# Optimization experiments

Hardware: AMD Instinct MI355X
Metric: run time of the kernel (lower is better)

## Reference

```python
import jax, jax.numpy as jnp
from jax import lax
import numpy as np

B, H, W = 16, 512, 512
OPENING_R, EROSION_R, DILATION_R = 5, 2, 1
MIN_SIZE, AREA_THRESHOLD = 2000, 300
INF = np.int32(2 ** 30)


def _disk(r):
    # skimage.morphology.disk: x^2 + y^2 <= r^2 on a (2r+1)^2 grid
    y, x = np.mgrid[-r:r + 1, -r:r + 1]
    return jnp.asarray((x * x + y * y <= r * r).astype(np.float32))


D_OPEN, D_ERODE, D_DILATE = _disk(OPENING_R), _disk(EROSION_R), _disk(DILATION_R)


def _conv2(x, k):
    return lax.conv_general_dilated(x[None, None], k[None, None], (1, 1), 'VALID')[0, 0]


def _erode(fg, se):
    # skimage binary_erosion uses border_value=True (image border does not erode)
    r = se.shape[0] // 2
    x = jnp.pad(fg.astype(jnp.float32), r, constant_values=1.0)
    return _conv2(x, se) >= se.sum() - 0.5


def _dilate(fg, se):
    # skimage binary_dilation uses border_value=False
    r = se.shape[0] // 2
    x = jnp.pad(fg.astype(jnp.float32), r, constant_values=0.0)
    return _conv2(x, se) > 0.5


def _seg_cummin(v, reset, axis, reverse):
    # segmented cumulative-min: scan resets wherever `reset` is True (background)
    def comb(a, b):
        av, af = a
        bv, bf = b
        return jnp.where(bf, bv, jnp.minimum(av, bv)), af | bf

    vv, _ = lax.associative_scan(comb, (v, reset), axis=axis, reverse=reverse)
    return vv


def _label(fg):
    # 4-connectivity connected-component labeling via min-label propagation.
    # Each fg pixel starts with its raveled index; alternating row/col segmented
    # cummin sweeps run under while_loop until a fixed point (root id per comp).
    h, w = fg.shape
    idx = jnp.arange(h * w, dtype=jnp.int32).reshape(h, w)
    lab0 = jnp.where(fg, idx, INF)
    bg = ~fg

    def sweep(l):
        for axis in (1, 0):
            for rev in (False, True):
                l = jnp.where(fg, _seg_cummin(l, bg, axis, rev), INF)
        return l

    def body(c):
        l, _ = c
        nl = sweep(l)
        return nl, jnp.array_equal(nl, l)

    lab, _ = lax.while_loop(lambda c: ~c[1], body, (lab0, jnp.array(False)))
    seg = jnp.where(fg, lab, 0).ravel()
    sizes = jax.ops.segment_sum(fg.astype(jnp.int32).ravel(), seg, num_segments=h * w)
    ncomp = jnp.sum(sizes > 0)
    return lab, sizes, ncomp


def _remove_small_objects(fg, min_size, guard):
    lab, sizes, ncomp = _label(fg)
    px = sizes[jnp.where(fg, lab, 0)]  # component size at every fg pixel
    kept = fg & (px >= min_size)
    # original only removes small objects when label(...).max() > 1
    return jnp.where(ncomp > 1, kept, fg) if guard else kept


def _pipeline(mask):
    fg = mask > 0
    fg = _remove_small_objects(fg, MIN_SIZE, True)
    # remove_small_holes == ~remove_small_objects(~fg, area_threshold + 1)
    fg = ~_remove_small_objects(~fg, AREA_THRESHOLD + 1, False)
    fg = _erode(fg, D_ERODE)
    fg = _dilate(_erode(fg, D_OPEN), D_OPEN)  # binary_opening
    fg = _remove_small_objects(fg, MIN_SIZE, True)
    fg = _dilate(fg, D_DILATE)
    return fg.astype(jnp.float32)  # original casts to int; float32 kept for vjp parity


def setup_inputs() -> dict:
    key = jax.random.key(0)
    # blobby binary masks: threshold bilinearly-upsampled low-res noise so that
    # realistic large connected components (> min_size px) exist
    low = jax.random.uniform(key, (B, H // 16, W // 16), dtype=jnp.float32)
    blob = jax.image.resize(low, (B, H, W), method='bilinear')
    return {'inputs': (blob > 0.5).astype(jnp.float32)}


def reference(inputs):
    return jax.vmap(_pipeline)(inputs)
```

## Files before the change

kernel.cpp:

```cpp
#include <hip/hip_runtime.h>
#include <stdint.h>

#define BATCH 16
#define H 512
#define W 512
#define HW (H * W)
#define NTOT (BATCH * HW)
#define NWORDS (NTOT / 64)

#define SROWS 16
#define SWORDS 128
#define SPIX 8192
#define NSTRIPS (NWORDS / SWORDS)
#define IMG_STRIPS 32
#define NBOUND_IMG 248

#define SPIN_LIMIT (1 << 20)

__device__ __forceinline__ int ald(const int* p) {
    return __hip_atomic_load((int*)p, __ATOMIC_RELAXED, __HIP_MEMORY_SCOPE_AGENT);
}
__device__ __forceinline__ void ast(int* p, int v) {
    __hip_atomic_store(p, v, __ATOMIC_RELAXED, __HIP_MEMORY_SCOPE_AGENT);
}
__device__ __forceinline__ uint64_t ald64(const uint64_t* p) {
    return __hip_atomic_load((uint64_t*)p, __ATOMIC_RELAXED, __HIP_MEMORY_SCOPE_AGENT);
}
__device__ __forceinline__ void ast64(uint64_t* p, uint64_t v) {
    __hip_atomic_store(p, v, __ATOMIC_RELAXED, __HIP_MEMORY_SCOPE_AGENT);
}

__device__ __forceinline__ int find_root_c(int* L, int x) {
    int r = x, p = ald(&L[r]);
    while (p != r) { r = p; p = ald(&L[r]); }
    if (ald(&L[x]) != r) atomicMin(&L[x], r);
    return r;
}

__device__ void merge_uf(int* L, int a, int b) {
    while (true) {
        a = find_root_c(L, a);
        b = find_root_c(L, b);
        if (a == b) return;
        int lo = a < b ? a : b;
        int hi = a < b ? b : a;
        int old = atomicMin(&L[hi], lo);
        if (old == hi) return;
        a = lo; b = old;
    }
}

__device__ __forceinline__ int find_root_lds(int* P, int x) {
    int r = x, p = P[r];
    while (p != r) { r = p; p = P[r]; }
    return r;
}

__device__ void merge_lds(int* P, int a, int b) {
    while (true) {
        a = find_root_lds(P, a);
        b = find_root_lds(P, b);
        if (a == b) return;
        int lo = a < b ? a : b;
        int hi = a < b ? b : a;
        int old = atomicMin(&P[hi], lo);
        if (old == hi) return;
        a = lo; b = old;
    }
}

__device__ __forceinline__ int start_of(uint64_t m, int i, int cv, int base) {
    uint64_t below = i ? ((~m) & ((1ull << i) - 1)) : 0ull;
    if (below == 0) return (cv >= 0) ? cv : base;
    int hz = 63 - __builtin_clzll(below);
    return base + hz + 1;
}

__device__ uint64_t keep_word(const uint64_t* __restrict__ bits,
                              const int* __restrict__ carry, const int* __restrict__ L,
                              const int* __restrict__ sizes, const int* __restrict__ ncomp,
                              int minsz, int gw) {
    uint64_t m = ald64(&bits[gw]);
    uint64_t res = m;
    if (m && ald(&ncomp[gw >> 12]) > 1) {
        int cv = ald(&carry[gw]);
        int base = gw << 6;
        while (m) {
            int s = __builtin_ctzll(m);
            uint64_t rest = m >> s;
            uint64_t nr = ~rest;
            int len = nr ? __builtin_ctzll(nr) : (64 - s);
            uint64_t piece = ((len >= 64) ? ~0ull : ((1ull << len) - 1)) << s;
            int start = (s == 0 && cv >= 0) ? cv : (base + s);
            if (ald(&sizes[ald(&L[start])]) < minsz) res &= ~piece;
            m &= ~piece;
        }
    }
    return res;
}

__device__ uint64_t fill_word(const uint64_t* __restrict__ bits,
                              const int* __restrict__ carry, const int* __restrict__ L,
                              const int* __restrict__ sizes, int minsz, int gw) {
    uint64_t fg = ald64(&bits[gw]);
    uint64_t bg = ~fg;
    uint64_t res = fg;
    int cv = ald(&carry[gw]);
    int base = gw << 6;
    while (bg) {
        int s = __builtin_ctzll(bg);
        uint64_t rest = bg >> s;
        uint64_t nr = ~rest;
        int len = nr ? __builtin_ctzll(nr) : (64 - s);
        uint64_t piece = ((len >= 64) ? ~0ull : ((1ull << len) - 1)) << s;
        int start = (s == 0 && cv >= 0) ? cv : (base + s);
        if (ald(&sizes[ald(&L[start])]) < minsz) res |= piece;
        bg &= ~piece;
    }
    return res;
}

template <int R, bool ERODE>
__device__ uint64_t morph_word_lds(const uint64_t* buf, int lrow, int w, int gyTop) {
    const uint64_t BORDER = ERODE ? ~0ull : 0ull;
    uint64_t res = ERODE ? ~0ull : 0ull;
#pragma unroll
    for (int dy = -R; dy <= R; ++dy) {
        int lr = lrow + dy;
        int gy = gyTop + lr;
        if (gy < 0 || gy >= H) continue;
        int v = R * R - dy * dy;
        int kx = 0;
        while ((kx + 1) * (kx + 1) <= v) ++kx;
        uint64_t cur = buf[lr * 8 + w];
        uint64_t prv = (w > 0) ? buf[lr * 8 + w - 1] : BORDER;
        uint64_t nxt = (w < 7) ? buf[lr * 8 + w + 1] : BORDER;
        uint64_t acc = cur;
#pragma unroll
        for (int dx = 1; dx <= kx; ++dx) {
            uint64_t right = (cur >> dx) | (nxt << (64 - dx));
            uint64_t left  = (cur << dx) | (prv >> (64 - dx));
            if (ERODE) acc &= right & left;
            else       acc |= right | left;
        }
        if (ERODE) res &= acc;
        else       res |= acc;
    }
    return res;
}

__device__ void strip_ccl_body(uint64_t m, uint64_t* sw, int* scarry, int* par,
                               int blk, int t,
                               int* __restrict__ carry, int* __restrict__ L,
                               int* __restrict__ sizes, int* __restrict__ ncomp) {
    if (t < SWORDS) sw[t] = m;
    __syncthreads();

    if (t < SROWS) {
        int cv = -1;
        for (int i = 0; i < 8; ++i) {
            int lw = t * 8 + i;
            scarry[lw] = cv;
            uint64_t w = sw[lw];
            if (w >> 63) {
                uint64_t z = ~w;
                if (z == 0) { if (cv < 0) cv = lw << 6; }
                else { int hz = 63 - __builtin_clzll(z); cv = (lw << 6) + hz + 1; }
            } else cv = -1;
        }
    }
    __syncthreads();

    int lbase = t << 6;
    int cv = -1;
    uint64_t starts = 0ull;
    if (t < SWORDS) {
        cv = scarry[t];
        ast(&carry[blk * SWORDS + t], (cv >= 0) ? (blk * SPIX + cv) : -1);
        starts = m & ~((m << 1) | ((cv >= 0) ? 1ull : 0ull));
        uint64_t ss = starts;
        while (ss) {
            int s = __builtin_ctzll(ss);
            par[lbase + s] = lbase + s;
            ss &= ss - 1;
        }
    }
    __syncthreads();

    if (t >= 8 && t < SWORDS && m) {
        uint64_t up = sw[t - 8];
        uint64_t cand = m & up;
        if (cand) {
            uint64_t curprev = (t & 7) ? sw[t - 1] : 0ull;
            uint64_t upprev  = (t & 7) ? sw[t - 9] : 0ull;
            uint64_t curl = (m << 1) | (curprev >> 63);
            uint64_t upl  = (up << 1) | (upprev >> 63);
            cand &= ~(curl & upl);
            int cvu = scarry[t - 8];
            while (cand) {
                int i = __builtin_ctzll(cand);
                int sP = start_of(m, i, cv, lbase);
                int sQ = start_of(up, i, cvu, lbase - 512);
                merge_lds(par, sP, sQ);
                cand &= cand - 1;
            }
        }
    }
    __syncthreads();

    if (t < SWORDS) {
        int gpix = blk * SPIX;
        uint64_t ss = starts;
        while (ss) {
            int s = __builtin_ctzll(ss);
            int ls = lbase + s;
            int r = find_root_lds(par, ls);
            ast(&L[gpix + ls], gpix + r);
            if (r == ls) ast(&sizes[gpix + ls], 0);
            ss &= ss - 1;
        }
    }
    if (t == 0 && (blk & 31) == 0) ast(&ncomp[blk >> 5], 0);
}

__device__ void merge_bound_item(const uint64_t* __restrict__ bits, uint64_t inv64,
                                 const int* __restrict__ carry, int* __restrict__ L,
                                 int gw, int w) {
    uint64_t cur = ald64(&bits[gw]) ^ inv64;
    uint64_t up  = ald64(&bits[gw - 8]) ^ inv64;
    uint64_t cand = cur & up;
    if (!cand) return;
    uint64_t curprev = w ? (ald64(&bits[gw - 1]) ^ inv64) : 0ull;
    uint64_t upprev  = w ? (ald64(&bits[gw - 9]) ^ inv64) : 0ull;
    uint64_t curl = (cur << 1) | (curprev >> 63);
    uint64_t upl  = (up << 1)  | (upprev >> 63);
    cand &= ~(curl & upl);
    if (!cand) return;
    int cvc = ald(&carry[gw]), cvu = ald(&carry[gw - 8]);
    int base = gw << 6;
    while (cand) {
        int i = __builtin_ctzll(cand);
        int sP = start_of(cur, i, cvc, base);
        int sQ = start_of(up, i, cvu, base - W);
        merge_uf(L, sP, sQ);
        cand &= cand - 1;
    }
}

__device__ void flatten_block(const uint64_t* __restrict__ bits, uint64_t inv64,
                              const int* __restrict__ carry, int* __restrict__ L,
                              int* __restrict__ sizes, int* __restrict__ ncomp,
                              int blk, int t, int* hk, int* hv) {
    if (t < 128) { hk[t] = -1; hv[t] = 0; }
    __syncthreads();
    if (t < SWORDS) {
        int gw = blk * SWORDS + t;
        uint64_t m = ald64(&bits[gw]) ^ inv64;
        if (m) {
            int cv = ald(&carry[gw]);
            int base = gw << 6;
            while (m) {
                int s = __builtin_ctzll(m);
                uint64_t rest = m >> s;
                uint64_t nr = ~rest;
                int len = nr ? __builtin_ctzll(nr) : (64 - s);
                uint64_t piece = ((len >= 64) ? ~0ull : ((1ull << len) - 1)) << s;
                bool initial = !(s == 0 && cv >= 0);
                int start = initial ? (base + s) : cv;
                int r = find_root_c(L, start);
                if (initial && r == start) atomicAdd(&ncomp[gw >> 12], 1);
                int cnt = __popcll(piece);
                uint32_t h = ((uint32_t)r * 2654435761u) >> 25;
                bool done = false;
                for (int tt = 0; tt < 16; ++tt) {
                    int slot = (h + tt) & 127;
                    int k = hk[slot];
                    if (k == -1) k = atomicCAS(&hk[slot], -1, r);
                    if (k == -1 || k == r) { atomicAdd(&hv[slot], cnt); done = true; break; }
                }
                if (!done) atomicAdd(&sizes[r], cnt);
                m &= ~piece;
            }
        }
    }
    __syncthreads();
    if (t < 128 && hk[t] != -1) atomicAdd(&sizes[hk[t]], hv[t]);
}

__device__ void keep_dilate_seg(const uint64_t* __restrict__ bits,
                                const int* __restrict__ carry, const int* __restrict__ L,
                                const int* __restrict__ sizes, const int* __restrict__ ncomp,
                                float* __restrict__ out,
                                int img, int y0, int t, uint64_t* kb, uint64_t* db) {
    if (t < 80) {
        int lr = t >> 3;
        int w = t & 7;
        int gy = y0 - 1 + lr;
        uint64_t v = 0;
        if (gy >= 0 && gy < H)
            v = keep_word(bits, carry, L, sizes, ncomp, 2000, img * 4096 + gy * 8 + w);
        kb[t] = v;
    }
    __syncthreads();
    if (t < 64) {
        int r = t >> 3, w = t & 7;
        uint64_t cur = kb[(r + 1) * 8 + w];
        uint64_t up  = kb[r * 8 + w];
        uint64_t dn  = kb[(r + 2) * 8 + w];
        uint64_t prv = w ? kb[(r + 1) * 8 + w - 1] : 0ull;
        uint64_t nxt = (w < 7) ? kb[(r + 1) * 8 + w + 1] : 0ull;
        db[t] = cur | up | dn | (cur << 1) | (prv >> 63) | (cur >> 1) | (nxt << 63);
    }
    __syncthreads();

    int q0 = t * 16;
    uint64_t wd = db[q0 >> 6];
    int sh = q0 & 63;
    float4* o = (float4*)(out + (size_t)img * HW + (size_t)y0 * W + q0);
#pragma unroll
    for (int k = 0; k < 4; ++k) {
        uint32_t nib = (uint32_t)(wd >> (sh + k * 4)) & 0xFu;
        float4 f;
        f.x = (nib & 1u) ? 1.0f : 0.0f;
        f.y = (nib & 2u) ? 1.0f : 0.0f;
        f.z = (nib & 4u) ? 1.0f : 0.0f;
        f.w = (nib & 8u) ? 1.0f : 0.0f;
        o[k] = f;
    }
}

__device__ __forceinline__ void ibar(int* flags, int img, int si, int phase) {
    int* base = flags + img * 32;
    __syncthreads();
    if (threadIdx.x == 0) {
        asm volatile("s_waitcnt vmcnt(0)" ::: "memory");
        ast(&base[si], phase);
    }
    if (threadIdx.x < 32) {
        int spins = 0;
        while (ald(&base[threadIdx.x]) < phase && ++spins < SPIN_LIMIT)
            __builtin_amdgcn_s_sleep(1);
    }
    __syncthreads();
}

__global__ __launch_bounds__(256, 2) void k_mega(
        const float4* __restrict__ in4, float* __restrict__ out,
        int* LA, int* sizesA, int* LB, int* sizesB,
        uint64_t* bits1, uint64_t* bits2, uint64_t* bits3,
        int* carryA, int* carryB, int* ncompA, int* ncompB, int* flags) {
    __shared__ uint64_t sw[SWORDS];
    __shared__ int scarry[SWORDS];
    __shared__ union US {
        int par[SPIX];
        struct { uint64_t A[320]; uint64_t B[320]; } mo;
        struct { int hk[128]; int hv[128]; } ha;
        struct { uint64_t kb[80]; uint64_t db[64]; } kd;
    } U;
    int blk = blockIdx.x;
    int t = threadIdx.x;
    int img = blk >> 5, si = blk & 31;

#pragma unroll
    for (int it = 0; it < 8; ++it) {
        int q = blk * (SPIX / 4) + it * 256 + t;
        float4 v = in4[q];
        uint32_t nib = (v.x > 0.0f ? 1u : 0u) | (v.y > 0.0f ? 2u : 0u) |
                       (v.z > 0.0f ? 4u : 0u) | (v.w > 0.0f ? 8u : 0u);
        uint64_t val = (uint64_t)nib << (4 * (t & 15));
        val |= __shfl_xor(val, 1);
        val |= __shfl_xor(val, 2);
        val |= __shfl_xor(val, 4);
        val |= __shfl_xor(val, 8);
        if ((t & 15) == 0) ast64(&bits1[q >> 4], val);
    }
    __syncthreads();

    {
        uint64_t m = (t < SWORDS) ? ald64(&bits1[blk * SWORDS + t]) : 0ull;
        strip_ccl_body(m, sw, scarry, U.par, blk, t, carryA, LA, sizesA, ncompA);
    }
    ibar(flags, img, si, 1);

    if (t < 8) {
        int item = si * 8 + t;
        if (item < NBOUND_IMG) {
            int gw = img * 4096 + ((item >> 3) + 1) * SROWS * 8 + (item & 7);
            merge_bound_item(bits1, 0ull, carryA, LA, gw, item & 7);
        }
    }
    ibar(flags, img, si, 2);

    flatten_block(bits1, 0ull, carryA, LA, sizesA, ncompA, blk, t, U.ha.hk, U.ha.hv);
    ibar(flags, img, si, 3);

    {
        uint64_t m = 0ull;
        if (t < SWORDS) {
            int gw = blk * SWORDS + t;
            uint64_t kw = keep_word(bits1, carryA, LA, sizesA, ncompA, 2000, gw);
            ast64(&bits2[gw], kw);
            m = ~kw;
        }
        strip_ccl_body(m, sw, scarry, U.par, blk, t, carryB, LB, sizesB, ncompB);
    }
    ibar(flags, img, si, 4);

    if (t < 8) {
        int item = si * 8 + t;
        if (item < NBOUND_IMG) {
            int gw = img * 4096 + ((item >> 3) + 1) * SROWS * 8 + (item & 7);
            merge_bound_item(bits2, ~0ull, carryB, LB, gw, item & 7);
        }
    }
    ibar(flags, img, si, 5);

    flatten_block(bits2, ~0ull, carryB, LB, sizesB, ncompB, blk, t, U.ha.hk, U.ha.hv);
    ibar(flags, img, si, 6);

    {
        int gyTop = si * 16 - 12;
        for (int lw = t; lw < 320; lw += 256) {
            int gy = gyTop + (lw >> 3);
            int w = lw & 7;
            uint64_t v = 0;
            if (gy >= 0 && gy < H)
                v = fill_word(bits2, carryB, LB, sizesB, 301, img * 4096 + gy * 8 + w);
            U.mo.A[lw] = v;
        }
        __syncthreads();
        for (int lw = t; lw < 320; lw += 256) {
            int lr = lw >> 3;
            if (lr >= 2 && lr <= 37) U.mo.B[lw] = morph_word_lds<2, true>(U.mo.A, lr, lw & 7, gyTop);
        }
        __syncthreads();
        for (int lw = t; lw < 320; lw += 256) {
            int lr = lw >> 3;
            if (lr >= 7 && lr <= 32) U.mo.A[lw] = morph_word_lds<5, true>(U.mo.B, lr, lw & 7, gyTop);
        }
        __syncthreads();
        for (int lw = t; lw < 320; lw += 256) {
            int lr = lw >> 3;
            if (lr >= 12 && lr <= 27) U.mo.B[lw] = morph_word_lds<5, false>(U.mo.A, lr, lw & 7, gyTop);
        }
        __syncthreads();
        uint64_t m3 = 0ull;
        if (t < SWORDS) {
            m3 = U.mo.B[t + 96];
            ast64(&bits3[blk * SWORDS + t], m3);
        }
        strip_ccl_body(m3, sw, scarry, U.par, blk, t, carryA, LA, sizesA, ncompA);
    }
    ibar(flags, img, si, 7);

    if (t < 8) {
        int item = si * 8 + t;
        if (item < NBOUND_IMG) {
            int gw = img * 4096 + ((item >> 3) + 1) * SROWS * 8 + (item & 7);
            merge_bound_item(bits3, 0ull, carryA, LA, gw, item & 7);
        }
    }
    ibar(flags, img, si, 8);

    flatten_block(bits3, 0ull, carryA, LA, sizesA, ncompA, blk, t, U.ha.hk, U.ha.hv);
    ibar(flags, img, si, 9);

    for (int k = 0; k < 2; ++k) {
        int seg = blk * 2 + k;
        int s8 = seg & 63;
        keep_dilate_seg(bits3, carryA, LA, sizesA, ncompA, out,
                        img, s8 * 8, t, U.kd.kb, U.kd.db);
        __syncthreads();
    }
}

extern "C" void kernel_launch(void* const* d_in, const int* in_sizes, int n_in,
                              void* d_out, int out_size, void* d_ws, size_t ws_size,
                              hipStream_t stream) {
    const float* in = (const float*)d_in[0];
    float* out = (float*)d_out;

    uint8_t* ws = (uint8_t*)d_ws;
    int* LA      = (int*)ws;
    int* sizesA  = (int*)(ws + (size_t)NTOT * 4);
    int* LB      = (int*)(ws + (size_t)NTOT * 8);
    int* sizesB  = (int*)(ws + (size_t)NTOT * 12);
    uint64_t* bits1 = (uint64_t*)(ws + (size_t)NTOT * 16);
    uint64_t* bits2 = bits1 + NWORDS;
    uint64_t* bits3 = bits2 + NWORDS;
    int* carryA = (int*)(bits3 + NWORDS);
    int* carryB = carryA + NWORDS;
    int* ncompA = carryB + NWORDS;
    int* ncompB = ncompA + BATCH;
    int* flags  = ncompB + BATCH;

    hipMemsetAsync(flags, 0, BATCH * 32 * sizeof(int), stream);

    k_mega<<<NSTRIPS, 256, 0, stream>>>((const float4*)in, out,
                                        LA, sizesA, LB, sizesB,
                                        bits1, bits2, bits3,
                                        carryA, carryB, ncompA, ncompB, flags);
}
```

Measured before the change: 192.9 us.

## Index union-find by compact run IDs instead of pixel indices

Labels each horizontal run in a strip with a dense run index, computed by a per-word run count and a block-wide prefix scan, and stores a per-word run base. The union-find parent array and the global L/sizes arrays are indexed by run ID, not raw pixel position. This shrinks the LDS parent array from 8192 to 4096 entries and the global label arrays, which could improve occupancy and cache footprint. In exchange it adds a 7-step scan with extra barriers, a wordrun array to read on every lookup, and a fixed cap of 4096 runs per strip that would overflow on pathological inputs.

```diff
diff --git a/kernel.cpp b/kernel.cpp
--- a/kernel.cpp
+++ b/kernel.cpp
@@ -14,6 +14,9 @@
 #define NSTRIPS (NWORDS / SWORDS)
 #define IMG_STRIPS 32
 #define NBOUND_IMG 248
+
+#define MAXR 4096
+#define NR (NSTRIPS * MAXR)
 
 #define SPIN_LIMIT (1 << 20)
 
@@ -69,30 +72,41 @@
     }
 }
 
-__device__ __forceinline__ int start_of(uint64_t m, int i, int cv, int base) {
+__device__ __forceinline__ int run_of(uint64_t m, int i, int cvrid, int wr) {
     uint64_t below = i ? ((~m) & ((1ull << i) - 1)) : 0ull;
-    if (below == 0) return (cv >= 0) ? cv : base;
-    int hz = 63 - __builtin_clzll(below);
-    return base + hz + 1;
+    if (below == 0) return (cvrid >= 0) ? cvrid : wr;
+    int s = 64 - __builtin_clzll(below);
+    uint64_t starts = m & ~((m << 1) | ((cvrid >= 0) ? 1ull : 0ull));
+    return wr + __popcll(starts & ((1ull << s) - 1));
+}
+
+__device__ __forceinline__ int run_of_lds(uint64_t m, int i, int cvrid,
+                                          uint64_t starts, int wb) {
+    uint64_t below = i ? ((~m) & ((1ull << i) - 1)) : 0ull;
+    if (below == 0) return (cvrid >= 0) ? cvrid : wb;
+    int s = 64 - __builtin_clzll(below);
+    return wb + __popcll(starts & ((1ull << s) - 1));
 }
 
 __device__ uint64_t keep_word(const uint64_t* __restrict__ bits,
-                              const int* __restrict__ carry, const int* __restrict__ L,
-                              const int* __restrict__ sizes, const int* __restrict__ ncomp,
-                              int minsz, int gw) {
+                              const int* __restrict__ carry, const int* __restrict__ wordrun,
+                              const int* __restrict__ L, const int* __restrict__ sizes,
+                              const int* __restrict__ ncomp, int minsz, int gw) {
     uint64_t m = ald64(&bits[gw]);
     uint64_t res = m;
     if (m && ald(&ncomp[gw >> 12]) > 1) {
         int cv = ald(&carry[gw]);
-        int base = gw << 6;
+        int wr = ald(&wordrun[gw]);
+        int rk = 0;
         while (m) {
             int s = __builtin_ctzll(m);
             uint64_t rest = m >> s;
             uint64_t nr = ~rest;
             int len = nr ? __builtin_ctzll(nr) : (64 - s);
             uint64_t piece = ((len >= 64) ? ~0ull : ((1ull << len) - 1)) << s;
-            int start = (s == 0 && cv >= 0) ? cv : (base + s);
-            if (ald(&sizes[ald(&L[start])]) < minsz) res &= ~piece;
+            bool initial = !(s == 0 && cv >= 0);
+            int rid = initial ? (wr + rk++) : cv;
+            if (ald(&sizes[ald(&L[rid])]) < minsz) res &= ~piece;
             m &= ~piece;
         }
     }
@@ -100,21 +114,24 @@
 }
 
 __device__ uint64_t fill_word(const uint64_t* __restrict__ bits,
-                              const int* __restrict__ carry, const int* __restrict__ L,
-                              const int* __restrict__ sizes, int minsz, int gw) {
+                              const int* __restrict__ carry, const int* __restrict__ wordrun,
+                              const int* __restrict__ L, const int* __restrict__ sizes,
+                              int minsz, int gw) {
     uint64_t fg = ald64(&bits[gw]);
     uint64_t bg = ~fg;
     uint64_t res = fg;
     int cv = ald(&carry[gw]);
-    int base = gw << 6;
+    int wr = ald(&wordrun[gw]);
+    int rk = 0;
     while (bg) {
         int s = __builtin_ctzll(bg);
         uint64_t rest = bg >> s;
         uint64_t nr = ~rest;
         int len = nr ? __builtin_ctzll(nr) : (64 - s);
         uint64_t piece = ((len >= 64) ? ~0ull : ((1ull << len) - 1)) << s;
-        int start = (s == 0 && cv >= 0) ? cv : (base + s);
-        if (ald(&sizes[ald(&L[start])]) < minsz) res |= piece;
+        bool initial = !(s == 0 && cv >= 0);
+        int rid = initial ? (wr + rk++) : cv;
+        if (ald(&sizes[ald(&L[rid])]) < minsz) res |= piece;
         bg &= ~piece;
     }
     return res;
@@ -149,12 +166,30 @@
     return res;
 }
 
-__device__ void strip_ccl_body(uint64_t m, uint64_t* sw, int* scarry, int* par,
+__device__ void strip_ccl_body(uint64_t m, uint64_t* sw, int* scarry,
+                               int* cntL, int* wbL, int* par,
                                int blk, int t,
-                               int* __restrict__ carry, int* __restrict__ L,
-                               int* __restrict__ sizes, int* __restrict__ ncomp) {
+                               int* __restrict__ carry, int* __restrict__ wordrun,
+                               int* __restrict__ L, int* __restrict__ sizes,
+                               int* __restrict__ ncomp) {
     if (t < SWORDS) sw[t] = m;
     __syncthreads();
+
+    if (t < SWORDS) {
+        bool cont = (t & 7) ? ((sw[t - 1] >> 63) != 0) : false;
+        int c = __popcll(m & ~(m << 1));
+        if ((m & 1ull) && cont) --c;
+        cntL[t] = c;
+        wbL[t] = c;
+    }
+    __syncthreads();
+    for (int off = 1; off < SWORDS; off <<= 1) {
+        int v = 0;
+        if (t < SWORDS && t >= off) v = wbL[t - off];
+        __syncthreads();
+        if (t < SWORDS) wbL[t] += v;
+        __syncthreads();
+    }
 
     if (t < SROWS) {
         int cv = -1;
@@ -162,28 +197,21 @@
             int lw = t * 8 + i;
             scarry[lw] = cv;
             uint64_t w = sw[lw];
-            if (w >> 63) {
-                uint64_t z = ~w;
-                if (z == 0) { if (cv < 0) cv = lw << 6; }
-                else { int hz = 63 - __builtin_clzll(z); cv = (lw << 6) + hz + 1; }
-            } else cv = -1;
-        }
-    }
-    __syncthreads();
-
-    int lbase = t << 6;
-    int cv = -1;
+            if (w >> 63) { if (cntL[lw] > 0) cv = wbL[lw] - 1; }
+            else cv = -1;
+        }
+    }
+    for (int i = t; i < MAXR; i += 256) par[i] = i;
+    __syncthreads();
+
+    int cv = -1, wb = 0;
     uint64_t starts = 0ull;
     if (t < SWORDS) {
         cv = scarry[t];
-        ast(&carry[blk * SWORDS + t], (cv >= 0) ? (blk * SPIX + cv) : -1);
+        wb = wbL[t] - cntL[t];
+        ast(&carry[blk * SWORDS + t], (cv >= 0) ? (blk * MAXR + cv) : -1);
+        ast(&wordrun[blk * SWORDS + t], blk * MAXR + wb);
         starts = m & ~((m << 1) | ((cv >= 0) ? 1ull : 0ull));
-        uint64_t ss = starts;
-        while (ss) {
-            int s = __builtin_ctzll(ss);
-            par[lbase + s] = lbase + s;
-            ss &= ss - 1;
-        }
     }
     __syncthreads();
 
@@ -197,10 +225,12 @@
             uint64_t upl  = (up << 1) | (upprev >> 63);
             cand &= ~(curl & upl);
             int cvu = scarry[t - 8];
+            int wbu = wbL[t - 8] - cntL[t - 8];
+            uint64_t startsU = up & ~((up << 1) | ((cvu >= 0) ? 1ull : 0ull));
             while (cand) {
                 int i = __builtin_ctzll(cand);
-                int sP = start_of(m, i, cv, lbase);
-                int sQ = start_of(up, i, cvu, lbase - 512);
+                int sP = run_of_lds(m, i, cv, starts, wb);
+                int sQ = run_of_lds(up, i, cvu, startsU, wbu);
                 merge_lds(par, sP, sQ);
                 cand &= cand - 1;
             }
@@ -209,14 +239,14 @@
     __syncthreads();
 
     if (t < SWORDS) {
-        int gpix = blk * SPIX;
+        int g = blk * MAXR;
         uint64_t ss = starts;
+        int rk = 0;
         while (ss) {
-            int s = __builtin_ctzll(ss);
-            int ls = lbase + s;
-            int r = find_root_lds(par, ls);
-            ast(&L[gpix + ls], gpix + r);
-            if (r == ls) ast(&sizes[gpix + ls], 0);
+            int rid = wb + rk; ++rk;
+            int r = find_root_lds(par, rid);
+            ast(&L[g + rid], g + r);
+            if (r == rid) ast(&sizes[g + rid], 0);
             ss &= ss - 1;
         }
     }
@@ -224,8 +254,9 @@
 }
 
 __device__ void merge_bound_item(const uint64_t* __restrict__ bits, uint64_t inv64,
-                                 const int* __restrict__ carry, int* __restrict__ L,
-                                 int gw, int w) {
+                                 const int* __restrict__ carry,
+                                 const int* __restrict__ wordrun,
+                                 int* __restrict__ L, int gw, int w) {
     uint64_t cur = ald64(&bits[gw]) ^ inv64;
     uint64_t up  = ald64(&bits[gw - 8]) ^ inv64;
     uint64_t cand = cur & up;
@@ -237,18 +268,20 @@
     cand &= ~(curl & upl);
     if (!cand) return;
     int cvc = ald(&carry[gw]), cvu = ald(&carry[gw - 8]);
-    int base = gw << 6;
+    int wrc = ald(&wordrun[gw]), wru = ald(&wordrun[gw - 8]);
     while (cand) {
         int i = __builtin_ctzll(cand);
-        int sP = start_of(cur, i, cvc, base);
-        int sQ = start_of(up, i, cvu, base - W);
+        int sP = run_of(cur, i, cvc, wrc);
+        int sQ = run_of(up, i, cvu, wru);
         merge_uf(L, sP, sQ);
         cand &= cand - 1;
     }
 }
 
 __device__ void flatten_block(const uint64_t* __restrict__ bits, uint64_t inv64,
-                              const int* __restrict__ carry, int* __restrict__ L,
+                              const int* __restrict__ carry,
+                              const int* __restrict__ wordrun,
+                              int* __restrict__ L,
                               int* __restrict__ sizes, int* __restrict__ ncomp,
                               int blk, int t, int* hk, int* hv) {
     if (t < 128) { hk[t] = -1; hv[t] = 0; }
@@ -258,7 +291,8 @@
         uint64_t m = ald64(&bits[gw]) ^ inv64;
         if (m) {
             int cv = ald(&carry[gw]);
-            int base = gw << 6;
+            int wr = ald(&wordrun[gw]);
+            int rk = 0;
             while (m) {
                 int s = __builtin_ctzll(m);
                 uint64_t rest = m >> s;
@@ -266,9 +300,9 @@
                 int len = nr ? __builtin_ctzll(nr) : (64 - s);
                 uint64_t piece = ((len >= 64) ? ~0ull : ((1ull << len) - 1)) << s;
                 bool initial = !(s == 0 && cv >= 0);
-                int start = initial ? (base + s) : cv;
-                int r = find_root_c(L, start);
-                if (initial && r == start) atomicAdd(&ncomp[gw >> 12], 1);
+                int rid = initial ? (wr + rk++) : cv;
+                int r = find_root_c(L, rid);
+                if (initial && r == rid) atomicAdd(&ncomp[gw >> 12], 1);
                 int cnt = __popcll(piece);
                 uint32_t h = ((uint32_t)r * 2654435761u) >> 25;
                 bool done = false;
@@ -288,8 +322,11 @@
 }
 
 __device__ void keep_dilate_seg(const uint64_t* __restrict__ bits,
-                                const int* __restrict__ carry, const int* __restrict__ L,
-                                const int* __restrict__ sizes, const int* __restrict__ ncomp,
+                                const int* __restrict__ carry,
+                                const int* __restrict__ wordrun,
+                                const int* __restrict__ L,
+                                const int* __restrict__ sizes,
+                                const int* __restrict__ ncomp,
                                 float* __restrict__ out,
                                 int img, int y0, int t, uint64_t* kb, uint64_t* db) {
     if (t < 80) {
@@ -298,7 +335,8 @@
         int gy = y0 - 1 + lr;
         uint64_t v = 0;
         if (gy >= 0 && gy < H)
-            v = keep_word(bits, carry, L, sizes, ncomp, 2000, img * 4096 + gy * 8 + w);
+            v = keep_word(bits, carry, wordrun, L, sizes, ncomp, 2000,
+                          img * 4096 + gy * 8 + w);
         kb[t] = v;
     }
     __syncthreads();
@@ -348,11 +386,14 @@
         const float4* __restrict__ in4, float* __restrict__ out,
         int* LA, int* sizesA, int* LB, int* sizesB,
         uint64_t* bits1, uint64_t* bits2, uint64_t* bits3,
-        int* carryA, int* carryB, int* ncompA, int* ncompB, int* flags) {
+        int* carryA, int* carryB, int* wordrunA, int* wordrunB,
+        int* ncompA, int* ncompB, int* flags) {
     __shared__ uint64_t sw[SWORDS];
     __shared__ int scarry[SWORDS];
+    __shared__ int cntL[SWORDS];
+    __shared__ int wbL[SWORDS];
     __shared__ union US {
-        int par[SPIX];
+        int par[MAXR];
         struct { uint64_t A[320]; uint64_t B[320]; } mo;
         struct { int hk[128]; int hv[128]; } ha;
         struct { uint64_t kb[80]; uint64_t db[64]; } kd;
@@ -378,7 +419,8 @@
 
     {
         uint64_t m = (t < SWORDS) ? ald64(&bits1[blk * SWORDS + t]) : 0ull;
-        strip_ccl_body(m, sw, scarry, U.par, blk, t, carryA, LA, sizesA, ncompA);
+        strip_ccl_body(m, sw, scarry, cntL, wbL, U.par, blk, t,
+                       carryA, wordrunA, LA, sizesA, ncompA);
     }
     ibar(flags, img, si, 1);
 
@@ -386,23 +428,26 @@
         int item = si * 8 + t;
         if (item < NBOUND_IMG) {
             int gw = img * 4096 + ((item >> 3) + 1) * SROWS * 8 + (item & 7);
-            merge_bound_item(bits1, 0ull, carryA, LA, gw, item & 7);
+            merge_bound_item(bits1, 0ull, carryA, wordrunA, LA, gw, item & 7);
         }
     }
     ibar(flags, img, si, 2);
 
-    flatten_block(bits1, 0ull, carryA, LA, sizesA, ncompA, blk, t, U.ha.hk, U.ha.hv);
+    flatten_block(bits1, 0ull, carryA, wordrunA, LA, sizesA, ncompA,
+                  blk, t, U.ha.hk, U.ha.hv);
     ibar(flags, img, si, 3);
 
     {
         uint64_t m = 0ull;
         if (t < SWORDS) {
             int gw = blk * SWORDS + t;
-            uint64_t kw = keep_word(bits1, carryA, LA, sizesA, ncompA, 2000, gw);
+            uint64_t kw = keep_word(bits1, carryA, wordrunA, LA, sizesA, ncompA,
+                                    2000, gw);
             ast64(&bits2[gw], kw);
             m = ~kw;
         }
-        strip_ccl_body(m, sw, scarry, U.par, blk, t, carryB, LB, sizesB, ncompB);
+        strip_ccl_body(m, sw, scarry, cntL, wbL, U.par, blk, t,
+                       carryB, wordrunB, LB, sizesB, ncompB);
     }
     ibar(flags, img, si, 4);
 
@@ -410,12 +455,13 @@
         int item = si * 8 + t;
         if (item < NBOUND_IMG) {
             int gw = img * 4096 + ((item >> 3) + 1) * SROWS * 8 + (item & 7);
-            merge_bound_item(bits2, ~0ull, carryB, LB, gw, item & 7);
+            merge_bound_item(bits2, ~0ull, carryB, wordrunB, LB, gw, item & 7);
         }
     }
     ibar(flags, img, si, 5);
 
-    flatten_block(bits2, ~0ull, carryB, LB, sizesB, ncompB, blk, t, U.ha.hk, U.ha.hv);
+    flatten_block(bits2, ~0ull, carryB, wordrunB, LB, sizesB, ncompB,
+                  blk, t, U.ha.hk, U.ha.hv);
     ibar(flags, img, si, 6);
 
     {
@@ -425,7 +471,8 @@
             int w = lw & 7;
             uint64_t v = 0;
             if (gy >= 0 && gy < H)
-                v = fill_word(bits2, carryB, LB, sizesB, 301, img * 4096 + gy * 8 + w);
+                v = fill_word(bits2, carryB, wordrunB, LB, sizesB, 301,
+                              img * 4096 + gy * 8 + w);
             U.mo.A[lw] = v;
         }
         __syncthreads();
@@ -449,7 +496,8 @@
             m3 = U.mo.B[t + 96];
             ast64(&bits3[blk * SWORDS + t], m3);
         }
-        strip_ccl_body(m3, sw, scarry, U.par, blk, t, carryA, LA, sizesA, ncompA);
+        strip_ccl_body(m3, sw, scarry, cntL, wbL, U.par, blk, t,
+                       carryA, wordrunA, LA, sizesA, ncompA);
     }
     ibar(flags, img, si, 7);
 
@@ -457,18 +505,19 @@
         int item = si * 8 + t;
         if (item < NBOUND_IMG) {
             int gw = img * 4096 + ((item >> 3) + 1) * SROWS * 8 + (item & 7);
-            merge_bound_item(bits3, 0ull, carryA, LA, gw, item & 7);
+            merge_bound_item(bits3, 0ull, carryA, wordrunA, LA, gw, item & 7);
         }
     }
     ibar(flags, img, si, 8);
 
-    flatten_block(bits3, 0ull, carryA, LA, sizesA, ncompA, blk, t, U.ha.hk, U.ha.hv);
+    flatten_block(bits3, 0ull, carryA, wordrunA, LA, sizesA, ncompA,
+                  blk, t, U.ha.hk, U.ha.hv);
     ibar(flags, img, si, 9);
 
     for (int k = 0; k < 2; ++k) {
         int seg = blk * 2 + k;
         int s8 = seg & 63;
-        keep_dilate_seg(bits3, carryA, LA, sizesA, ncompA, out,
+        keep_dilate_seg(bits3, carryA, wordrunA, LA, sizesA, ncompA, out,
                         img, s8 * 8, t, U.kd.kb, U.kd.db);
         __syncthreads();
     }
@@ -482,22 +531,25 @@
 
     uint8_t* ws = (uint8_t*)d_ws;
     int* LA      = (int*)ws;
-    int* sizesA  = (int*)(ws + (size_t)NTOT * 4);
-    int* LB      = (int*)(ws + (size_t)NTOT * 8);
-    int* sizesB  = (int*)(ws + (size_t)NTOT * 12);
-    uint64_t* bits1 = (uint64_t*)(ws + (size_t)NTOT * 16);
+    int* sizesA  = LA + NR;
+    int* LB      = sizesA + NR;
+    int* sizesB  = LB + NR;
+    uint64_t* bits1 = (uint64_t*)(sizesB + NR);
     uint64_t* bits2 = bits1 + NWORDS;
     uint64_t* bits3 = bits2 + NWORDS;
-    int* carryA = (int*)(bits3 + NWORDS);
-    int* carryB = carryA + NWORDS;
-    int* ncompA = carryB + NWORDS;
-    int* ncompB = ncompA + BATCH;
-    int* flags  = ncompB + BATCH;
+    int* carryA   = (int*)(bits3 + NWORDS);
+    int* carryB   = carryA + NWORDS;
+    int* wordrunA = carryB + NWORDS;
+    int* wordrunB = wordrunA + NWORDS;
+    int* ncompA   = wordrunB + NWORDS;
+    int* ncompB   = ncompA + BATCH;
+    int* flags    = ncompB + BATCH;
 
     hipMemsetAsync(flags, 0, BATCH * 32 * sizeof(int), stream);
 
     k_mega<<<NSTRIPS, 256, 0, stream>>>((const float4*)in, out,
                                         LA, sizesA, LB, sizesB,
                                         bits1, bits2, bits3,
-                                        carryA, carryB, ncompA, ncompB, flags);
-}
+                                        carryA, carryB, wordrunA, wordrunB,
+                                        ncompA, ncompB, flags);
+}
```

After: 186.9 us. 3.1% less time.
